# Kernel tuning notes

Hardware: AMD Instinct MI355X
Metric: run time of the kernel (lower is better)

The kernel has to match this reference:

```python
import jax, jax.numpy as jnp
import numpy as np

N, D, S, C, H = 65536, 512, 32, 64, 64  # batch, input_size, n_subnets, cols/subnet, hidden
GROUP = 32  # columns per predictor group


def _build_col_ids():
    # 16 groups of 32 cols; interactions = (i,i+1) and (i,i+2) mod 16
    pairs = [(i, (i + 1) % 16) for i in range(16)] + [(i, (i + 2) % 16) for i in range(16)]
    ids = np.array([np.concatenate([np.arange(a * GROUP, (a + 1) * GROUP),
                                    np.arange(b * GROUP, (b + 1) * GROUP)])
                    for a, b in pairs], dtype=np.int32)  # [S, C]
    return jnp.asarray(ids)


def setup_inputs() -> dict:
    key = jax.random.key(0)
    ks = jax.random.split(key, 7)
    scale = 0.05  # keep log_rate inside clamp range most of the time
    return {
        "x": jax.random.normal(ks[0], (N, D), jnp.float32),
        "skip_w": jax.random.normal(ks[1], (D,), jnp.float32) * scale,
        "skip_b": jax.random.normal(ks[2], (1,), jnp.float32) * scale,
        "W1": jax.random.normal(ks[3], (S, C, H), jnp.float32) * scale,
        "b1": jax.random.normal(ks[4], (S, H), jnp.float32) * scale,
        "W2": jax.random.normal(ks[5], (S, H), jnp.float32) * scale,
        "b2": jax.random.normal(ks[6], (S,), jnp.float32) * scale,
        "col_ids": _build_col_ids(),
    }


def reference(x, skip_w, skip_b, W1, b1, W2, b2, col_ids):
    # skip: Linear(D,1) then squeeze -> [N]
    log_rate = x @ skip_w + skip_b[0]
    # fused gather + batched tiny MLP over all S subnets
    xg = x[:, col_ids]                                  # [N, S, C]
    h = jax.nn.relu(jnp.einsum('nsc,sch->nsh', xg, W1) + b1)  # [N, S, H]
    out = jnp.einsum('nsh,sh->ns', h, W2) + b2          # [N, S]
    log_rate = log_rate + out.sum(axis=-1)
    return jnp.clip(log_rate, -20.0, 20.0)
```

## Files before the change

kernel.cpp:

```cpp
#include <hip/hip_runtime.h>

#define NROWS 65536
#define DCOLS 512

typedef float  f32x4  __attribute__((ext_vector_type(4)));
typedef __bf16 bf16x8 __attribute__((ext_vector_type(8)));

__device__ __forceinline__ unsigned short f2bf(float f) {
    unsigned int u = __builtin_bit_cast(unsigned int, f);
    u += 0x7fffu + ((u >> 16) & 1u);
    return (unsigned short)(u >> 16);
}

__global__ void pack_kernel(const float* __restrict__ W1,
                            const float* __restrict__ b1,
                            const float* __restrict__ W2,
                            unsigned short* __restrict__ w1p,
                            float2* __restrict__ pk) {
    int idx  = blockIdx.x * 256 + threadIdx.x;
    int j    = idx & 7;
    int lane = (idx >> 3) & 63;
    int f    = (idx >> 9) & 7;
    int s    = idx >> 12;
    int kt = f >> 2, nt = f & 3;
    int c = kt * 32 + (lane >> 4) * 8 + j;
    int h = nt * 16 + (lane & 15);
    w1p[idx] = f2bf(W1[(s * 64 + c) * 64 + h]);
    if (idx < 2048) pk[idx] = make_float2(b1[idx], W2[idx]);
}

__launch_bounds__(256, 2)
__global__ void fused_kernel(const float* __restrict__ x,
                             const float* __restrict__ skip_w,
                             const float* __restrict__ skip_b,
                             const float* __restrict__ b2,
                             const unsigned short* __restrict__ w1p,
                             const float2* __restrict__ pk,
                             float* __restrict__ out) {
    __shared__ uint4 w1buf[2][512];

    const int tid  = threadIdx.x;
    const int wave = tid >> 6;
    const int lane = tid & 63;
    const int m    = lane & 15;
    const int q    = lane >> 4;
    const int row0 = blockIdx.x * 128 + wave * 32;

    uint4 afr[2][16];
    float sp[2] = {0.f, 0.f};
#pragma unroll
    for (int g = 0; g < 16; ++g) {
        const float4 sw0 = *(const float4*)(skip_w + g * 32 + q * 8);
        const float4 sw1 = *(const float4*)(skip_w + g * 32 + q * 8 + 4);
#pragma unroll
        for (int mt = 0; mt < 2; ++mt) {
            const float* xp = x + (long)(row0 + mt * 16 + m) * DCOLS + g * 32 + q * 8;
            const float4 a0 = *(const float4*)(xp);
            const float4 a1 = *(const float4*)(xp + 4);
            float s0 = fmaf(a0.x, sw0.x, fmaf(a0.y, sw0.y, fmaf(a0.z, sw0.z, a0.w * sw0.w)));
            float s1 = fmaf(a1.x, sw1.x, fmaf(a1.y, sw1.y, fmaf(a1.z, sw1.z, a1.w * sw1.w)));
            sp[mt] += s0 + s1;
            unsigned int u01 = (unsigned int)f2bf(a0.x) | ((unsigned int)f2bf(a0.y) << 16);
            unsigned int u23 = (unsigned int)f2bf(a0.z) | ((unsigned int)f2bf(a0.w) << 16);
            unsigned int u45 = (unsigned int)f2bf(a1.x) | ((unsigned int)f2bf(a1.y) << 16);
            unsigned int u67 = (unsigned int)f2bf(a1.z) | ((unsigned int)f2bf(a1.w) << 16);
            afr[mt][g] = make_uint4(u01, u23, u45, u67);
        }
    }
    float sf[2];
#pragma unroll
    for (int mt = 0; mt < 2; ++mt) {
        float v = sp[mt];
        v += __shfl_xor(v, 16);
        v += __shfl_xor(v, 32);
        sf[mt] = v;
    }

    float b2s = 0.f;
#pragma unroll
    for (int i = 0; i < 32; ++i) b2s += b2[i];
    const float sb0 = skip_b[0];

    const uint4* wp = (const uint4*)w1p;
    float part[2][4] = {{0.f,0.f,0.f,0.f},{0.f,0.f,0.f,0.f}};

    w1buf[0][tid]       = wp[tid];
    w1buf[0][tid + 256] = wp[tid + 256];
    __syncthreads();

#pragma unroll
    for (int s = 0; s < 32; ++s) {
        const int cb = s & 1, nb = cb ^ 1;
        if (s + 1 < 32) {
            w1buf[nb][tid]       = wp[(s + 1) * 512 + tid];
            w1buf[nb][tid + 256] = wp[(s + 1) * 512 + tid + 256];
        }
        const int ga = s & 15;
        const int gb = ((s & 15) + 1 + (s >> 4)) & 15;

        bf16x8 bfr[2][4];
#pragma unroll
        for (int kt = 0; kt < 2; ++kt)
#pragma unroll
            for (int nt = 0; nt < 4; ++nt)
                bfr[kt][nt] = __builtin_bit_cast(bf16x8, w1buf[cb][(kt * 4 + nt) * 64 + lane]);

        f32x4 acc[2][4];
#pragma unroll
        for (int mt = 0; mt < 2; ++mt) {
            const bf16x8 a0 = __builtin_bit_cast(bf16x8, afr[mt][ga]);
            const bf16x8 a1 = __builtin_bit_cast(bf16x8, afr[mt][gb]);
#pragma unroll
            for (int nt = 0; nt < 4; ++nt) {
                f32x4 z = {0.f, 0.f, 0.f, 0.f};
                acc[mt][nt] = __builtin_amdgcn_mfma_f32_16x16x32_bf16(a0, bfr[0][nt], z, 0, 0, 0);
                acc[mt][nt] = __builtin_amdgcn_mfma_f32_16x16x32_bf16(a1, bfr[1][nt], acc[mt][nt], 0, 0, 0);
            }
        }

#pragma unroll
        for (int nt = 0; nt < 4; ++nt) {
            const float2 bw = pk[s * 64 + nt * 16 + m];
#pragma unroll
            for (int mt = 0; mt < 2; ++mt)
#pragma unroll
                for (int r = 0; r < 4; ++r) {
                    float h = acc[mt][nt][r] + bw.x;
                    h = fmaxf(h, 0.f);
                    part[mt][r] = fmaf(h, bw.y, part[mt][r]);
                }
        }
        __syncthreads();
    }

#pragma unroll
    for (int mt = 0; mt < 2; ++mt)
#pragma unroll
        for (int r = 0; r < 4; ++r) {
            float v = part[mt][r];
            v += __shfl_xor(v, 1);
            v += __shfl_xor(v, 2);
            v += __shfl_xor(v, 4);
            v += __shfl_xor(v, 8);
            const float skipv = __shfl(sf[mt], q * 4 + r);
            float val = v + b2s + sb0 + skipv;
            val = fminf(fmaxf(val, -20.f), 20.f);
            if (m == 0) out[row0 + mt * 16 + q * 4 + r] = val;
        }
}

extern "C" void kernel_launch(void* const* d_in, const int* in_sizes, int n_in,
                              void* d_out, int out_size, void* d_ws, size_t ws_size,
                              hipStream_t stream) {
    const float* x      = (const float*)d_in[0];
    const float* skip_w = (const float*)d_in[1];
    const float* skip_b = (const float*)d_in[2];
    const float* W1     = (const float*)d_in[3];
    const float* b1     = (const float*)d_in[4];
    const float* W2     = (const float*)d_in[5];
    const float* b2     = (const float*)d_in[6];

    unsigned short* w1p = (unsigned short*)d_ws;
    float2* pk = (float2*)((char*)d_ws + 262144);

    pack_kernel<<<512, 256, 0, stream>>>(W1, b1, W2, w1p, pk);
    fused_kernel<<<NROWS / 128, 256, 0, stream>>>(x, skip_w, skip_b, b2, w1p, pk,
                                                  (float*)d_out);
}
```

Measured before the change: 224.9 us.

## Halve rows per wave to raise occupancy and fix LDS prefetch race

Each wave now handles 16 rows instead of 32, which halves the A-fragment register array, and launch bounds are raised to 4 blocks per CU with twice as many blocks. The W1 prefetch is loaded into registers first and written to LDS after a barrier, adding a second __syncthreads per subnet. bf16 packing now uses the library paired conversion. In exchange, each W1 tile read from LDS is reused across half as many rows, so W1 global/LDS traffic per row doubles and there are more barriers.

```diff
diff --git a/kernel.cpp b/kernel.cpp
--- a/kernel.cpp
+++ b/kernel.cpp
@@ -1,4 +1,5 @@
 #include <hip/hip_runtime.h>
+#include <hip/hip_bf16.h>
 
 #define NROWS 65536
 #define DCOLS 512
@@ -10,6 +11,13 @@
     unsigned int u = __builtin_bit_cast(unsigned int, f);
     u += 0x7fffu + ((u >> 16) & 1u);
     return (unsigned short)(u >> 16);
+}
+
+__device__ __forceinline__ unsigned int pkbf(float lo, float hi) {
+    __hip_bfloat162 t = __float22bfloat162_rn(make_float2(lo, hi));
+    unsigned int u;
+    __builtin_memcpy(&u, &t, 4);
+    return u;
 }
 
 __global__ void pack_kernel(const float* __restrict__ W1,
@@ -29,7 +37,7 @@
     if (idx < 2048) pk[idx] = make_float2(b1[idx], W2[idx]);
 }
 
-__launch_bounds__(256, 2)
+__launch_bounds__(256, 4)
 __global__ void fused_kernel(const float* __restrict__ x,
                              const float* __restrict__ skip_w,
                              const float* __restrict__ skip_b,
@@ -44,37 +52,26 @@
     const int lane = tid & 63;
     const int m    = lane & 15;
     const int q    = lane >> 4;
-    const int row0 = blockIdx.x * 128 + wave * 32;
+    const int row0 = blockIdx.x * 64 + wave * 16;
 
-    uint4 afr[2][16];
-    float sp[2] = {0.f, 0.f};
+    uint4 afr[16];
+    float sp = 0.f;
+    const float* xrow = x + (long)(row0 + m) * DCOLS;
 #pragma unroll
     for (int g = 0; g < 16; ++g) {
         const float4 sw0 = *(const float4*)(skip_w + g * 32 + q * 8);
         const float4 sw1 = *(const float4*)(skip_w + g * 32 + q * 8 + 4);
-#pragma unroll
-        for (int mt = 0; mt < 2; ++mt) {
-            const float* xp = x + (long)(row0 + mt * 16 + m) * DCOLS + g * 32 + q * 8;
-            const float4 a0 = *(const float4*)(xp);
-            const float4 a1 = *(const float4*)(xp + 4);
-            float s0 = fmaf(a0.x, sw0.x, fmaf(a0.y, sw0.y, fmaf(a0.z, sw0.z, a0.w * sw0.w)));
-            float s1 = fmaf(a1.x, sw1.x, fmaf(a1.y, sw1.y, fmaf(a1.z, sw1.z, a1.w * sw1.w)));
-            sp[mt] += s0 + s1;
-            unsigned int u01 = (unsigned int)f2bf(a0.x) | ((unsigned int)f2bf(a0.y) << 16);
-            unsigned int u23 = (unsigned int)f2bf(a0.z) | ((unsigned int)f2bf(a0.w) << 16);
-            unsigned int u45 = (unsigned int)f2bf(a1.x) | ((unsigned int)f2bf(a1.y) << 16);
-            unsigned int u67 = (unsigned int)f2bf(a1.z) | ((unsigned int)f2bf(a1.w) << 16);
-            afr[mt][g] = make_uint4(u01, u23, u45, u67);
-        }
+        const float4 a0  = *(const float4*)(xrow + g * 32 + q * 8);
+        const float4 a1  = *(const float4*)(xrow + g * 32 + q * 8 + 4);
+        sp = fmaf(a0.x, sw0.x, fmaf(a0.y, sw0.y, fmaf(a0.z, sw0.z, fmaf(a0.w, sw0.w, sp))));
+        sp = fmaf(a1.x, sw1.x, fmaf(a1.y, sw1.y, fmaf(a1.z, sw1.z, fmaf(a1.w, sw1.w, sp))));
+        afr[g] = make_uint4(pkbf(a0.x, a0.y), pkbf(a0.z, a0.w),
+                            pkbf(a1.x, a1.y), pkbf(a1.z, a1.w));
     }
-    float sf[2];
-#pragma unroll
-    for (int mt = 0; mt < 2; ++mt) {
-        float v = sp[mt];
-        v += __shfl_xor(v, 16);
-        v += __shfl_xor(v, 32);
-        sf[mt] = v;
-    }
+    float v = sp;
+    v += __shfl_xor(v, 16);
+    v += __shfl_xor(v, 32);
+    const float sf = v;
 
     float b2s = 0.f;
 #pragma unroll
@@ -82,7 +79,7 @@
     const float sb0 = skip_b[0];
 
     const uint4* wp = (const uint4*)w1p;
-    float part[2][4] = {{0.f,0.f,0.f,0.f},{0.f,0.f,0.f,0.f}};
+    float part[4] = {0.f, 0.f, 0.f, 0.f};
 
     w1buf[0][tid]       = wp[tid];
     w1buf[0][tid + 256] = wp[tid + 256];
@@ -91,62 +88,59 @@
 #pragma unroll
     for (int s = 0; s < 32; ++s) {
         const int cb = s & 1, nb = cb ^ 1;
+        uint4 pf0, pf1;
         if (s + 1 < 32) {
-            w1buf[nb][tid]       = wp[(s + 1) * 512 + tid];
-            w1buf[nb][tid + 256] = wp[(s + 1) * 512 + tid + 256];
+            pf0 = wp[(s + 1) * 512 + tid];
+            pf1 = wp[(s + 1) * 512 + tid + 256];
         }
         const int ga = s & 15;
         const int gb = ((s & 15) + 1 + (s >> 4)) & 15;
+        const bf16x8 a0 = __builtin_bit_cast(bf16x8, afr[ga]);
+        const bf16x8 a1 = __builtin_bit_cast(bf16x8, afr[gb]);
 
-        bf16x8 bfr[2][4];
+        f32x4 acc[4];
 #pragma unroll
-        for (int kt = 0; kt < 2; ++kt)
+        for (int nt = 0; nt < 4; ++nt) {
+            const bf16x8 b0 = __builtin_bit_cast(bf16x8, w1buf[cb][nt * 64 + lane]);
+            f32x4 z = {0.f, 0.f, 0.f, 0.f};
+            acc[nt] = __builtin_amdgcn_mfma_f32_16x16x32_bf16(a0, b0, z, 0, 0, 0);
+        }
 #pragma unroll
-            for (int nt = 0; nt < 4; ++nt)
-                bfr[kt][nt] = __builtin_bit_cast(bf16x8, w1buf[cb][(kt * 4 + nt) * 64 + lane]);
-
-        f32x4 acc[2][4];
-#pragma unroll
-        for (int mt = 0; mt < 2; ++mt) {
-            const bf16x8 a0 = __builtin_bit_cast(bf16x8, afr[mt][ga]);
-            const bf16x8 a1 = __builtin_bit_cast(bf16x8, afr[mt][gb]);
-#pragma unroll
-            for (int nt = 0; nt < 4; ++nt) {
-                f32x4 z = {0.f, 0.f, 0.f, 0.f};
-                acc[mt][nt] = __builtin_amdgcn_mfma_f32_16x16x32_bf16(a0, bfr[0][nt], z, 0, 0, 0);
-                acc[mt][nt] = __builtin_amdgcn_mfma_f32_16x16x32_bf16(a1, bfr[1][nt], acc[mt][nt], 0, 0, 0);
-            }
+        for (int nt = 0; nt < 4; ++nt) {
+            const bf16x8 b1f = __builtin_bit_cast(bf16x8, w1buf[cb][(4 + nt) * 64 + lane]);
+            acc[nt] = __builtin_amdgcn_mfma_f32_16x16x32_bf16(a1, b1f, acc[nt], 0, 0, 0);
         }
 
 #pragma unroll
         for (int nt = 0; nt < 4; ++nt) {
             const float2 bw = pk[s * 64 + nt * 16 + m];
 #pragma unroll
-            for (int mt = 0; mt < 2; ++mt)
-#pragma unroll
-                for (int r = 0; r < 4; ++r) {
-                    float h = acc[mt][nt][r] + bw.x;
-                    h = fmaxf(h, 0.f);
-                    part[mt][r] = fmaf(h, bw.y, part[mt][r]);
-                }
+            for (int r = 0; r < 4; ++r) {
+                float h = acc[nt][r] + bw.x;
+                h = fmaxf(h, 0.f);
+                part[r] = fmaf(h, bw.y, part[r]);
+            }
+        }
+        __syncthreads();
+        if (s + 1 < 32) {
+            w1buf[nb][tid]       = pf0;
+            w1buf[nb][tid + 256] = pf1;
         }
         __syncthreads();
     }
 
 #pragma unroll
-    for (int mt = 0; mt < 2; ++mt)
-#pragma unroll
-        for (int r = 0; r < 4; ++r) {
-            float v = part[mt][r];
-            v += __shfl_xor(v, 1);
-            v += __shfl_xor(v, 2);
-            v += __shfl_xor(v, 4);
-            v += __shfl_xor(v, 8);
-            const float skipv = __shfl(sf[mt], q * 4 + r);
-            float val = v + b2s + sb0 + skipv;
-            val = fminf(fmaxf(val, -20.f), 20.f);
-            if (m == 0) out[row0 + mt * 16 + q * 4 + r] = val;
-        }
+    for (int r = 0; r < 4; ++r) {
+        float t = part[r];
+        t += __shfl_xor(t, 1);
+        t += __shfl_xor(t, 2);
+        t += __shfl_xor(t, 4);
+        t += __shfl_xor(t, 8);
+        const float skipv = __shfl(sf, q * 4 + r);
+        float val = t + b2s + sb0 + skipv;
+        val = fminf(fmaxf(val, -20.f), 20.f);
+        if (m == 0) out[row0 + q * 4 + r] = val;
+    }
 }
 
 extern "C" void kernel_launch(void* const* d_in, const int* in_sizes, int n_in,
@@ -164,6 +158,6 @@
     float2* pk = (float2*)((char*)d_ws + 262144);
 
     pack_kernel<<<512, 256, 0, stream>>>(W1, b1, W2, w1p, pk);
-    fused_kernel<<<NROWS / 128, 256, 0, stream>>>(x, skip_w, skip_b, b2, w1p, pk,
-                                                  (float*)d_out);
+    fused_kernel<<<NROWS / 64, 256, 0, stream>>>(x, skip_w, skip_b, b2, w1p, pk,
+                                                 (float*)d_out);
 }
```

After: 239.1 us. +6.3%, slower.
